# Kernel optimization log

Hardware: AMD Instinct MI355X
Metric: run time of the kernel (lower is better)

Reference implementation:

```python
import jax, jax.numpy as jnp
import numpy as np

N = 50000
E = 800000
T = 12
HID = 128
K = 3
F_IN = 7  # 1 (x) + 4 (env) + 2 (coords)
CIN = F_IN + HID  # DCRNN concatenates input with hidden state


def setup_inputs() -> dict:
    key = jax.random.key(0)
    ks = jax.random.split(key, 16)
    inp = {
        "x": jax.random.normal(ks[0], (N, T), dtype=jnp.float32),
        "env": jax.random.normal(ks[1], (N, 4, T), dtype=jnp.float32),
        "coords": jax.random.uniform(ks[2], (N, 2), dtype=jnp.float32),
        "edge_index": jax.random.randint(ks[3], (2, E), 0, N, dtype=jnp.int32),
        "edge_weight": jax.random.uniform(ks[4], (E,), dtype=jnp.float32),
        "local_night": jax.random.uniform(ks[5], (N, T + 1), dtype=jnp.float32),
        # DCRNN gate diffusion-conv weights: [2 (out/in direction), K, Cin, Cout]
        "Wz": jax.random.normal(ks[6], (2, K, CIN, HID), dtype=jnp.float32) * 0.05,
        "bz": jnp.zeros((HID,), dtype=jnp.float32),
        "Wr": jax.random.normal(ks[7], (2, K, CIN, HID), dtype=jnp.float32) * 0.05,
        "br": jnp.zeros((HID,), dtype=jnp.float32),
        "Wh": jax.random.normal(ks[8], (2, K, CIN, HID), dtype=jnp.float32) * 0.05,
        "bh": jnp.zeros((HID,), dtype=jnp.float32),
        "lin_W": jax.random.normal(ks[9], (HID, 1), dtype=jnp.float32) * 0.05,
        "lin_b": jnp.zeros((1,), dtype=jnp.float32),
    }
    return inp


def reference(x, env, coords, edge_weight, local_night, Wz, bz, Wr, br, Wh, bh, lin_W, lin_b, edge_index):
    row, col = edge_index[0], edge_index[1]
    n = x.shape[0]

    # out/in degrees of the weighted adjacency A[row, col] = w
    deg_out = jax.ops.segment_sum(edge_weight, row, num_segments=n)
    deg_in = jax.ops.segment_sum(edge_weight, col, num_segments=n)
    inv_out = jnp.where(deg_out > 0, 1.0 / deg_out, 0.0)
    inv_in = jnp.where(deg_in > 0, 1.0 / deg_in, 0.0)

    def prop_out(v):  # (D_O^{-1} A) v : gather from col, scatter-add to row
        msg = edge_weight[:, None] * v[col]
        return inv_out[:, None] * jax.ops.segment_sum(msg, row, num_segments=n)

    def prop_in(v):  # (D_I^{-1} A^T) v : gather from row, scatter-add to col
        msg = edge_weight[:, None] * v[row]
        return inv_in[:, None] * jax.ops.segment_sum(msg, col, num_segments=n)

    def dconv(X, W, b):
        # K-hop bidirectional diffusion convolution
        H = X @ (W[0, 0] + W[1, 0])
        Tx0 = X
        Tx_o = prop_out(X)
        Tx_i = prop_in(X)
        H = H + Tx_o @ W[0, 1] + Tx_i @ W[1, 1]
        for k in range(2, W.shape[1]):
            Tx_o = 2.0 * prop_out(Tx_o) - Tx0
            Tx_i = 2.0 * prop_in(Tx_i) - Tx0
            H = H + Tx_o @ W[0, k] + Tx_i @ W[1, k]
        return H + b

    env_t = jnp.moveaxis(env, -1, 0)          # [T, N, 4]
    night_t = jnp.transpose(local_night[:, 1:])  # [T, N]
    hid0 = jnp.zeros((n, HID), dtype=x.dtype)   # hidden state resets each call (H=None)

    def step(x_prev, ts):
        e, night = ts
        X = jnp.concatenate([x_prev, e, coords], axis=1)   # [N, 7]
        Xh = jnp.concatenate([X, hid0], axis=1)            # [N, 7+HID]
        Z = jax.nn.sigmoid(dconv(Xh, Wz, bz))
        R = jax.nn.sigmoid(dconv(Xh, Wr, br))  # H*R = 0 since H0 = 0; kept for fidelity
        H_tilde = jnp.tanh(dconv(Xh, Wh, bh))
        H_new = Z * hid0 + (1.0 - Z) * H_tilde
        out = jax.nn.relu(H_new) @ lin_W + lin_b           # [N, 1]
        out = out * night[:, None]
        return out, out

    x0 = x[:, 0:1]
    _, preds = jax.lax.scan(step, x0, (env_t, night_t))    # preds: [T, N, 1]
    predictions = jnp.concatenate([x0, jnp.transpose(preds[..., 0])], axis=1)  # [N, T+1]
    return predictions
```

## Files before the change

### kernel.cpp

```cpp
#include <hip/hip_runtime.h>
#include <hip/hip_fp16.h>

#define Nn 50000
#define Ee 800000
#define Tt 12
#define NBAND 8
#define BAND 6250
#define SCB 196

__global__ __launch_bounds__(256) void pack_hist_kernel(
    const int* __restrict__ ei, const float* __restrict__ ew,
    uint2* __restrict__ packed, int* __restrict__ cntR, int* __restrict__ cntC)
{
    int e = blockIdx.x * 256 + threadIdx.x;
    if (e >= Ee) return;
    int r = ei[e], c = ei[Ee + e];
    unsigned wb = __half_as_ushort(__float2half(ew[e]));
    packed[e] = make_uint2(((unsigned)c << 16) | wb, ((unsigned)r << 16) | wb);
    atomicAdd(&cntR[r], 1);
    atomicAdd(&cntC[c], 1);
}

__global__ __launch_bounds__(256) void scanA_kernel(
    const int* __restrict__ cntR, const int* __restrict__ cntC,
    int* __restrict__ bsum)
{
    const int* cnt = blockIdx.y ? cntC : cntR;
    int i = blockIdx.x * 256 + threadIdx.x;
    int v = (i < Nn) ? cnt[i] : 0;
    __shared__ int ws_[4];
    v += __shfl_xor(v, 1);  v += __shfl_xor(v, 2);  v += __shfl_xor(v, 4);
    v += __shfl_xor(v, 8);  v += __shfl_xor(v, 16); v += __shfl_xor(v, 32);
    if ((threadIdx.x & 63) == 0) ws_[threadIdx.x >> 6] = v;
    __syncthreads();
    if (threadIdx.x == 0)
        bsum[blockIdx.y * 256 + blockIdx.x] = ws_[0] + ws_[1] + ws_[2] + ws_[3];
}

__global__ __launch_bounds__(256) void scanB_kernel(
    const int* __restrict__ bsum, int* __restrict__ bbase)
{
    int y = blockIdx.x;
    __shared__ int s[256];
    int t = threadIdx.x;
    int v = (t < SCB) ? bsum[y * 256 + t] : 0;
    s[t] = v;
    __syncthreads();
    for (int off = 1; off < 256; off <<= 1) {
        int u = (t >= off) ? s[t - off] : 0;
        __syncthreads();
        s[t] += u;
        __syncthreads();
    }
    bbase[y * 256 + t] = s[t] - v;
}

__global__ __launch_bounds__(256) void scanC_kernel(
    const int* __restrict__ cntR, const int* __restrict__ cntC,
    const int* __restrict__ bbase,
    int* __restrict__ startR, int* __restrict__ startC,
    int* __restrict__ nextR, int* __restrict__ nextC)
{
    int y = blockIdx.y;
    const int* cnt = y ? cntC : cntR;
    int* start     = y ? startC : startR;
    int* nxt       = y ? nextC : nextR;
    int i = blockIdx.x * 256 + threadIdx.x;
    int v = (i < Nn) ? cnt[i] : 0;
    __shared__ int s[256];
    int t = threadIdx.x;
    s[t] = v;
    __syncthreads();
    for (int off = 1; off < 256; off <<= 1) {
        int u = (t >= off) ? s[t - off] : 0;
        __syncthreads();
        s[t] += u;
        __syncthreads();
    }
    int st = bbase[y * 256 + blockIdx.x] + s[t] - v;
    if (i < Nn) { start[i] = st; nxt[i] = st; }
}

__global__ __launch_bounds__(256) void scatter_banded(
    const uint2* __restrict__ packed,
    int* __restrict__ nextR, int* __restrict__ nextC,
    unsigned* __restrict__ adjR, unsigned* __restrict__ adjC)
{
    int band = blockIdx.x & (NBAND - 1);
    int chunk = blockIdx.x >> 3;
    int lo = band * BAND, hi = lo + BAND;
    int stride = (gridDim.x >> 3) * 256;
    for (int e = chunk * 256 + threadIdx.x; e < Ee; e += stride) {
        uint2 p = packed[e];
        int c = (int)(p.x >> 16);
        int r = (int)(p.y >> 16);
        if (r >= lo && r < hi) adjR[atomicAdd(&nextR[r], 1)] = p.x;
        if (c >= lo && c < hi) adjC[atomicAdd(&nextC[c], 1)] = p.y;
    }
}

__global__ __launch_bounds__(256) void weff_kernel(
    const float* __restrict__ Wz, const float* __restrict__ Wh,
    const float* __restrict__ bz, const float* __restrict__ bh,
    float* __restrict__ wzT, float* __restrict__ whT)
{
    int idx = blockIdx.x * 256 + threadIdx.x;
    if (idx >= 2 * 36 * 128) return;
    const float* W = (idx < 36 * 128) ? Wz : Wh;
    const float* B = (idx < 36 * 128) ? bz : bh;
    float* O       = (idx < 36 * 128) ? wzT : whT;
    int rem = idx % (36 * 128);
    int k = rem / 128, j = rem % 128;
    float v;
    if (k == 35) v = B[j];
    else {
        int p = k / 7, rr = k % 7;
        if (p == 0)      v = W[(0 * 135 + rr) * 128 + j] + W[(3 * 135 + rr) * 128 + j];
        else if (p == 1) v = W[(1 * 135 + rr) * 128 + j];
        else if (p == 2) v = W[(4 * 135 + rr) * 128 + j];
        else if (p == 3) v = W[(2 * 135 + rr) * 128 + j];
        else             v = W[(5 * 135 + rr) * 128 + j];
    }
    O[k * 128 + j] = v;
}

__global__ __launch_bounds__(256) void init_kernel(
    const float* __restrict__ x, const float* __restrict__ env,
    const float* __restrict__ coords, __half* __restrict__ Xh,
    float* __restrict__ out)
{
    int i = blockIdx.x * 256 + threadIdx.x;
    if (i >= Nn) return;
    float xv = x[i * Tt];
    __half* r = Xh + (long)i * 8;
    r[0] = __float2half(xv);
    #pragma unroll
    for (int c = 0; c < 4; c++) r[1 + c] = __float2half(env[i * 48 + c * 12]);
    r[5] = __float2half(coords[i * 2 + 0]);
    r[6] = __float2half(coords[i * 2 + 1]);
    r[7] = __half(0.f);
    out[i * 13 + 0] = xv;
}

__device__ __forceinline__ void unpack8(const __half* p, float* v) {
    uint4 hv = *((const uint4*)p);
    float2 p0 = __half22float2(*(__half2*)&hv.x);
    float2 p1 = __half22float2(*(__half2*)&hv.y);
    float2 p2 = __half22float2(*(__half2*)&hv.z);
    float2 p3 = __half22float2(*(__half2*)&hv.w);
    v[0] = p0.x; v[1] = p0.y; v[2] = p1.x; v[3] = p1.y;
    v[4] = p2.x; v[5] = p2.y; v[6] = p3.x;
}

__device__ __forceinline__ void pack8(__half* p, const float* v) {
    __half2 q0 = __floats2half2_rn(v[0], v[1]);
    __half2 q1 = __floats2half2_rn(v[2], v[3]);
    __half2 q2 = __floats2half2_rn(v[4], v[5]);
    __half2 q3 = __floats2half2_rn(v[6], 0.f);
    uint4 st;
    st.x = *(unsigned*)&q0; st.y = *(unsigned*)&q1;
    st.z = *(unsigned*)&q2; st.w = *(unsigned*)&q3;
    *((uint4*)p) = st;
}

__device__ __forceinline__ void acc7(float* a, float w, uint4 hv) {
    float2 p0 = __half22float2(*(__half2*)&hv.x);
    float2 p1 = __half22float2(*(__half2*)&hv.y);
    float2 p2 = __half22float2(*(__half2*)&hv.z);
    float2 p3 = __half22float2(*(__half2*)&hv.w);
    a[0] = fmaf(w, p0.x, a[0]); a[1] = fmaf(w, p0.y, a[1]);
    a[2] = fmaf(w, p1.x, a[2]); a[3] = fmaf(w, p1.y, a[3]);
    a[4] = fmaf(w, p2.x, a[4]); a[5] = fmaf(w, p2.y, a[5]);
    a[6] = fmaf(w, p3.x, a[6]);
}

__device__ __forceinline__ float wdec(unsigned ed) {
    return __half2float(__ushort_as_half((unsigned short)(ed & 0xffffu)));
}

__global__ __launch_bounds__(256) void gather1_kernel(
    const int* __restrict__ startR, const int* __restrict__ cntR,
    const unsigned* __restrict__ adjR,
    const int* __restrict__ startC, const int* __restrict__ cntC,
    const unsigned* __restrict__ adjC,
    const __half* __restrict__ Xh,
    __half* __restrict__ TxoH, __half* __restrict__ TxiH,
    float* __restrict__ inv_out, float* __restrict__ inv_in)
{
    int tid = blockIdx.x * 256 + threadIdx.x;
    if (tid >= Nn * 8) return;
    int node = tid >> 3;
    int dir = (tid >> 2) & 1, sub = tid & 3;
    const int*      st  = dir ? startC : startR;
    const int*      cn  = dir ? cntC : cntR;
    const unsigned* adj = dir ? adjC : adjR;
    int b = st[node], e = b + cn[node];
    float a[7] = {0.f, 0.f, 0.f, 0.f, 0.f, 0.f, 0.f};
    float sw = 0.f;
    int k = b + sub;
    for (; k + 12 < e; k += 16) {
        unsigned e0 = adj[k], e1 = adj[k + 4], e2 = adj[k + 8], e3 = adj[k + 12];
        uint4 r0 = *(const uint4*)(Xh + (long)(e0 >> 16) * 8);
        uint4 r1 = *(const uint4*)(Xh + (long)(e1 >> 16) * 8);
        uint4 r2 = *(const uint4*)(Xh + (long)(e2 >> 16) * 8);
        uint4 r3 = *(const uint4*)(Xh + (long)(e3 >> 16) * 8);
        float w0 = wdec(e0), w1 = wdec(e1), w2 = wdec(e2), w3 = wdec(e3);
        acc7(a, w0, r0); acc7(a, w1, r1); acc7(a, w2, r2); acc7(a, w3, r3);
        sw += (w0 + w1) + (w2 + w3);
    }
    for (; k < e; k += 4) {
        unsigned ed = adj[k];
        uint4 rv = *(const uint4*)(Xh + (long)(ed >> 16) * 8);
        float w = wdec(ed);
        acc7(a, w, rv);
        sw += w;
    }
    #pragma unroll
    for (int m = 1; m <= 2; m <<= 1) {
        #pragma unroll
        for (int q = 0; q < 7; q++) a[q] += __shfl_xor(a[q], m);
        sw += __shfl_xor(sw, m);
    }
    if (sub == 0) {
        float inv = sw > 0.f ? 1.f / sw : 0.f;
        (dir ? inv_in : inv_out)[node] = inv;
        #pragma unroll
        for (int q = 0; q < 7; q++) a[q] *= inv;
        pack8((dir ? TxiH : TxoH) + (long)node * 8, a);
    }
}

__global__ __launch_bounds__(256) void step2_kernel(
    const int* __restrict__ startR, const int* __restrict__ cntR,
    const unsigned* __restrict__ adjR,
    const int* __restrict__ startC, const int* __restrict__ cntC,
    const unsigned* __restrict__ adjC,
    const float* __restrict__ inv_out, const float* __restrict__ inv_in,
    const float* __restrict__ env, const float* __restrict__ night,
    const float* __restrict__ wzT, const float* __restrict__ whT,
    const float* __restrict__ linW, const float* __restrict__ linb,
    __half* __restrict__ Xh,
    const __half* __restrict__ TxoH, const __half* __restrict__ TxiH,
    float* __restrict__ out, int t)
{
    __shared__ float f_s[32][36];
    __shared__ float part_s[2][32];
    int tid = threadIdx.x;
    int base = blockIdx.x * 32;

    {
        int nl = tid >> 3;
        int dir = (tid >> 2) & 1, sub = tid & 3;
        int node = base + nl;
        int nc = node < Nn ? node : Nn - 1;
        const int*      st  = dir ? startC : startR;
        const int*      cn  = dir ? cntC : cntR;
        const unsigned* adj = dir ? adjC : adjR;
        const __half*   src = dir ? TxiH : TxoH;
        int b = st[nc], e = b + cn[nc];
        float a[7] = {0.f, 0.f, 0.f, 0.f, 0.f, 0.f, 0.f};
        int k = b + sub;
        for (; k + 12 < e; k += 16) {
            unsigned e0 = adj[k], e1 = adj[k + 4], e2 = adj[k + 8], e3 = adj[k + 12];
            uint4 r0 = *(const uint4*)(src + (long)(e0 >> 16) * 8);
            uint4 r1 = *(const uint4*)(src + (long)(e1 >> 16) * 8);
            uint4 r2 = *(const uint4*)(src + (long)(e2 >> 16) * 8);
            uint4 r3 = *(const uint4*)(src + (long)(e3 >> 16) * 8);
            float w0 = wdec(e0), w1 = wdec(e1), w2 = wdec(e2), w3 = wdec(e3);
            acc7(a, w0, r0); acc7(a, w1, r1); acc7(a, w2, r2); acc7(a, w3, r3);
        }
        for (; k < e; k += 4) {
            unsigned ed = adj[k];
            uint4 rv = *(const uint4*)(src + (long)(ed >> 16) * 8);
            acc7(a, wdec(ed), rv);
        }
        #pragma unroll
        for (int m = 1; m <= 2; m <<= 1) {
            #pragma unroll
            for (int q = 0; q < 7; q++) a[q] += __shfl_xor(a[q], m);
        }
        if (sub == 0) {
            float s2 = 2.f * (dir ? inv_in[nc] : inv_out[nc]);
            float xv[7], tx[7];
            unpack8(Xh + (long)nc * 8, xv);
            unpack8(src + (long)nc * 8, tx);
            #pragma unroll
            for (int q = 0; q < 7; q++) {
                f_s[nl][21 + 7 * dir + q] = fmaf(s2, a[q], -xv[q]);
                f_s[nl][7 + 7 * dir + q]  = tx[q];
            }
            if (dir == 0) {
                #pragma unroll
                for (int q = 0; q < 7; q++) f_s[nl][q] = xv[q];
                f_s[nl][35] = 1.f;
            }
        }
    }
    __syncthreads();

    int lane = tid & 63;
    int wave = tid >> 6;
    int chSel = wave & 1;
    int ch = chSel * 64 + lane;
    int half_id = wave >> 1;
    float wz[36], wh[36];
    #pragma unroll
    for (int k = 0; k < 36; k++) wz[k] = wzT[k * 128 + ch];
    #pragma unroll
    for (int k = 0; k < 36; k++) wh[k] = whT[k * 128 + ch];
    float lw = linW[ch];
    float lb = linb[0];

    #pragma unroll 1
    for (int n = 0; n < 16; n++) {
        int ni = half_id * 16 + n;
        const float4* fv = (const float4*)f_s[ni];
        float hz = 0.f, hh = 0.f;
        #pragma unroll
        for (int q = 0; q < 9; q++) {
            float4 fq = fv[q];
            hz = fmaf(fq.x, wz[q*4+0], hz); hh = fmaf(fq.x, wh[q*4+0], hh);
            hz = fmaf(fq.y, wz[q*4+1], hz); hh = fmaf(fq.y, wh[q*4+1], hh);
            hz = fmaf(fq.z, wz[q*4+2], hz); hh = fmaf(fq.z, wh[q*4+2], hh);
            hz = fmaf(fq.w, wz[q*4+3], hz); hh = fmaf(fq.w, wh[q*4+3], hh);
        }
        float z  = 1.f / (1.f + __expf(-hz));
        float e2 = __expf(2.f * hh);
        float ht = 1.f - 2.f / (e2 + 1.f);
        float v = fmaxf((1.f - z) * ht, 0.f) * lw;
        v += __shfl_xor(v, 1);  v += __shfl_xor(v, 2);  v += __shfl_xor(v, 4);
        v += __shfl_xor(v, 8);  v += __shfl_xor(v, 16); v += __shfl_xor(v, 32);
        if (lane == 0) part_s[chSel][ni] = v;
    }
    __syncthreads();
    if (tid < 32) {
        int node = base + tid;
        if (node < Nn) {
            float o = part_s[0][tid] + part_s[1][tid] + lb;
            o *= night[(long)node * 13 + t + 1];
            out[(long)node * 13 + t + 1] = o;
            if (t + 1 < Tt) {
                __half* xr = Xh + (long)node * 8;
                xr[0] = __float2half(o);
                #pragma unroll
                for (int c = 0; c < 4; c++)
                    xr[1 + c] = __float2half(env[(long)node * 48 + c * 12 + t + 1]);
            }
        }
    }
}

extern "C" void kernel_launch(void* const* d_in, const int* in_sizes, int n_in,
                              void* d_out, int out_size, void* d_ws, size_t ws_size,
                              hipStream_t stream) {
    const float* x      = (const float*)d_in[0];
    const float* env    = (const float*)d_in[1];
    const float* coords = (const float*)d_in[2];
    const int*   ei     = (const int*)d_in[3];
    const float* ew     = (const float*)d_in[4];
    const float* night  = (const float*)d_in[5];
    const float* Wz     = (const float*)d_in[6];
    const float* bz     = (const float*)d_in[7];
    const float* Wh     = (const float*)d_in[10];
    const float* bh     = (const float*)d_in[11];
    const float* linW   = (const float*)d_in[12];
    const float* linb   = (const float*)d_in[13];
    float* out = (float*)d_out;

    float* w = (float*)d_ws;
    float* wzT     = w;
    float* whT     = w + 4608;
    float* inv_out = w + 9216;
    float* inv_in  = w + 59216;
    __half* Xh   = (__half*)(w + 109216);
    __half* TxoH = (__half*)(w + 309216);
    __half* TxiH = (__half*)(w + 509216);
    int* cntR    = (int*)(w + 709216);
    int* cntC    = cntR + 50000;
    int* startR  = cntC + 50000;
    int* startC  = startR + 50000;
    int* nextR   = startC + 50000;
    int* nextC   = nextR + 50000;
    int* bsum    = nextC + 50000;
    int* bbase   = bsum + 512;
    uint2* packed  = (uint2*)(bbase + 512);
    unsigned* adjR = (unsigned*)(packed + Ee);
    unsigned* adjC = adjR + Ee;

    hipMemsetAsync(cntR, 0, 2 * Nn * sizeof(int), stream);
    pack_hist_kernel<<<(Ee + 255) / 256, 256, 0, stream>>>(ei, ew, packed, cntR, cntC);
    scanA_kernel<<<dim3(SCB, 2), 256, 0, stream>>>(cntR, cntC, bsum);
    scanB_kernel<<<2, 256, 0, stream>>>(bsum, bbase);
    scanC_kernel<<<dim3(SCB, 2), 256, 0, stream>>>(
        cntR, cntC, bbase, startR, startC, nextR, nextC);
    scatter_banded<<<8 * 256, 256, 0, stream>>>(packed, nextR, nextC, adjR, adjC);

    weff_kernel<<<(2 * 36 * 128 + 255) / 256, 256, 0, stream>>>(Wz, Wh, bz, bh, wzT, whT);
    init_kernel<<<(Nn + 255) / 256, 256, 0, stream>>>(x, env, coords, Xh, out);

    for (int t = 0; t < Tt; t++) {
        gather1_kernel<<<(Nn * 8 + 255) / 256, 256, 0, stream>>>(
            startR, cntR, adjR, startC, cntC, adjC, Xh, TxoH, TxiH, inv_out, inv_in);
        step2_kernel<<<(Nn + 31) / 32, 256, 0, stream>>>(
            startR, cntR, adjR, startC, cntC, adjC, inv_out, inv_in,
            env, night, wzT, whT, linW, linb, Xh, TxoH, TxiH, out, t);
    }
}
```

Measured before the change: 791.1 us.

## Use 8 lanes per node-direction in gathers, prefetch edges, nontemporal setup I/O

The gather kernels now use 8 threads per node and direction instead of 4. Each thread issues three predicated edge loads and row gathers up front, then loops over any remaining edges, which raises memory-level parallelism for the average degree of 16. The step2 kernel grows to 512-thread blocks so each wave handles 8 nodes in the dense gate phase. The setup kernels switch to nontemporal loads and stores, and the banded scatter is unrolled by 4. This costs more threads, an extra shuffle round, and possibly higher register pressure at 512-thread launch bounds with 72 weight registers.

```diff
diff --git a/kernel.cpp b/kernel.cpp
--- a/kernel.cpp
+++ b/kernel.cpp
@@ -14,9 +14,14 @@
 {
     int e = blockIdx.x * 256 + threadIdx.x;
     if (e >= Ee) return;
-    int r = ei[e], c = ei[Ee + e];
-    unsigned wb = __half_as_ushort(__float2half(ew[e]));
-    packed[e] = make_uint2(((unsigned)c << 16) | wb, ((unsigned)r << 16) | wb);
+    int r = __builtin_nontemporal_load(ei + e);
+    int c = __builtin_nontemporal_load(ei + Ee + e);
+    float w = __builtin_nontemporal_load(ew + e);
+    unsigned wb = __half_as_ushort(__float2half(w));
+    unsigned lo = ((unsigned)c << 16) | wb;
+    unsigned hi = ((unsigned)r << 16) | wb;
+    unsigned long long v = ((unsigned long long)hi << 32) | lo;
+    __builtin_nontemporal_store(v, (unsigned long long*)packed + e);
     atomicAdd(&cntR[r], 1);
     atomicAdd(&cntC[c], 1);
 }
@@ -88,14 +93,24 @@
 {
     int band = blockIdx.x & (NBAND - 1);
     int chunk = blockIdx.x >> 3;
-    int lo = band * BAND, hi = lo + BAND;
+    int blo = band * BAND, bhi = blo + BAND;
     int stride = (gridDim.x >> 3) * 256;
-    for (int e = chunk * 256 + threadIdx.x; e < Ee; e += stride) {
-        uint2 p = packed[e];
-        int c = (int)(p.x >> 16);
-        int r = (int)(p.y >> 16);
-        if (r >= lo && r < hi) adjR[atomicAdd(&nextR[r], 1)] = p.x;
-        if (c >= lo && c < hi) adjC[atomicAdd(&nextC[c], 1)] = p.y;
+    const unsigned long long* p64 = (const unsigned long long*)packed;
+    for (int e0 = chunk * 256 + threadIdx.x; e0 < Ee; e0 += 4 * stride) {
+        int e1 = e0 + stride, e2 = e0 + 2 * stride, e3 = e0 + 3 * stride;
+        bool g1 = e1 < Ee, g2 = e2 < Ee, g3 = e3 < Ee;
+        unsigned long long p0 = __builtin_nontemporal_load(p64 + e0);
+        unsigned long long p1 = __builtin_nontemporal_load(p64 + (g1 ? e1 : e0));
+        unsigned long long p2 = __builtin_nontemporal_load(p64 + (g2 ? e2 : e0));
+        unsigned long long p3 = __builtin_nontemporal_load(p64 + (g3 ? e3 : e0));
+        #define PROC(p, ok) do { if (ok) {                                     \
+            unsigned lo = (unsigned)(p); unsigned hi = (unsigned)((p) >> 32);  \
+            int c = (int)(lo >> 16), r = (int)(hi >> 16);                      \
+            if (r >= blo && r < bhi) adjR[atomicAdd(&nextR[r], 1)] = lo;       \
+            if (c >= blo && c < bhi) adjC[atomicAdd(&nextC[c], 1)] = hi;       \
+        } } while (0)
+        PROC(p0, true); PROC(p1, g1); PROC(p2, g2); PROC(p3, g3);
+        #undef PROC
     }
 }
 
@@ -188,27 +203,28 @@
     float* __restrict__ inv_out, float* __restrict__ inv_in)
 {
     int tid = blockIdx.x * 256 + threadIdx.x;
-    if (tid >= Nn * 8) return;
-    int node = tid >> 3;
-    int dir = (tid >> 2) & 1, sub = tid & 3;
+    int node = tid >> 4;
+    int dir = (tid >> 3) & 1, sub = tid & 7;
     const int*      st  = dir ? startC : startR;
     const int*      cn  = dir ? cntC : cntR;
     const unsigned* adj = dir ? adjC : adjR;
     int b = st[node], e = b + cn[node];
+    int safe = (b < e) ? b : 0;
+    int k0 = b + sub;
+    bool v0 = k0 < e, v1 = k0 + 8 < e, v2 = k0 + 16 < e;
+    unsigned e0 = adj[v0 ? k0 : safe];
+    unsigned e1 = adj[v1 ? k0 + 8 : safe];
+    unsigned e2 = adj[v2 ? k0 + 16 : safe];
+    uint4 r0 = *(const uint4*)(Xh + (long)(e0 >> 16) * 8);
+    uint4 r1 = *(const uint4*)(Xh + (long)(e1 >> 16) * 8);
+    uint4 r2 = *(const uint4*)(Xh + (long)(e2 >> 16) * 8);
+    float w0 = v0 ? wdec(e0) : 0.f;
+    float w1 = v1 ? wdec(e1) : 0.f;
+    float w2 = v2 ? wdec(e2) : 0.f;
     float a[7] = {0.f, 0.f, 0.f, 0.f, 0.f, 0.f, 0.f};
-    float sw = 0.f;
-    int k = b + sub;
-    for (; k + 12 < e; k += 16) {
-        unsigned e0 = adj[k], e1 = adj[k + 4], e2 = adj[k + 8], e3 = adj[k + 12];
-        uint4 r0 = *(const uint4*)(Xh + (long)(e0 >> 16) * 8);
-        uint4 r1 = *(const uint4*)(Xh + (long)(e1 >> 16) * 8);
-        uint4 r2 = *(const uint4*)(Xh + (long)(e2 >> 16) * 8);
-        uint4 r3 = *(const uint4*)(Xh + (long)(e3 >> 16) * 8);
-        float w0 = wdec(e0), w1 = wdec(e1), w2 = wdec(e2), w3 = wdec(e3);
-        acc7(a, w0, r0); acc7(a, w1, r1); acc7(a, w2, r2); acc7(a, w3, r3);
-        sw += (w0 + w1) + (w2 + w3);
-    }
-    for (; k < e; k += 4) {
+    acc7(a, w0, r0); acc7(a, w1, r1); acc7(a, w2, r2);
+    float sw = (w0 + w1) + w2;
+    for (int k = k0 + 24; k < e; k += 8) {
         unsigned ed = adj[k];
         uint4 rv = *(const uint4*)(Xh + (long)(ed >> 16) * 8);
         float w = wdec(ed);
@@ -216,7 +232,7 @@
         sw += w;
     }
     #pragma unroll
-    for (int m = 1; m <= 2; m <<= 1) {
+    for (int m = 1; m <= 4; m <<= 1) {
         #pragma unroll
         for (int q = 0; q < 7; q++) a[q] += __shfl_xor(a[q], m);
         sw += __shfl_xor(sw, m);
@@ -230,7 +246,7 @@
     }
 }
 
-__global__ __launch_bounds__(256) void step2_kernel(
+__global__ __launch_bounds__(512) void step2_kernel(
     const int* __restrict__ startR, const int* __restrict__ cntR,
     const unsigned* __restrict__ adjR,
     const int* __restrict__ startC, const int* __restrict__ cntC,
@@ -249,8 +265,8 @@
     int base = blockIdx.x * 32;
 
     {
-        int nl = tid >> 3;
-        int dir = (tid >> 2) & 1, sub = tid & 3;
+        int nl = tid >> 4;
+        int dir = (tid >> 3) & 1, sub = tid & 7;
         int node = base + nl;
         int nc = node < Nn ? node : Nn - 1;
         const int*      st  = dir ? startC : startR;
@@ -258,24 +274,27 @@
         const unsigned* adj = dir ? adjC : adjR;
         const __half*   src = dir ? TxiH : TxoH;
         int b = st[nc], e = b + cn[nc];
+        int safe = (b < e) ? b : 0;
+        int k0 = b + sub;
+        bool v0 = k0 < e, v1 = k0 + 8 < e, v2 = k0 + 16 < e;
+        unsigned e0 = adj[v0 ? k0 : safe];
+        unsigned e1 = adj[v1 ? k0 + 8 : safe];
+        unsigned e2 = adj[v2 ? k0 + 16 : safe];
+        uint4 r0 = *(const uint4*)(src + (long)(e0 >> 16) * 8);
+        uint4 r1 = *(const uint4*)(src + (long)(e1 >> 16) * 8);
+        uint4 r2 = *(const uint4*)(src + (long)(e2 >> 16) * 8);
+        float w0 = v0 ? wdec(e0) : 0.f;
+        float w1 = v1 ? wdec(e1) : 0.f;
+        float w2 = v2 ? wdec(e2) : 0.f;
         float a[7] = {0.f, 0.f, 0.f, 0.f, 0.f, 0.f, 0.f};
-        int k = b + sub;
-        for (; k + 12 < e; k += 16) {
-            unsigned e0 = adj[k], e1 = adj[k + 4], e2 = adj[k + 8], e3 = adj[k + 12];
-            uint4 r0 = *(const uint4*)(src + (long)(e0 >> 16) * 8);
-            uint4 r1 = *(const uint4*)(src + (long)(e1 >> 16) * 8);
-            uint4 r2 = *(const uint4*)(src + (long)(e2 >> 16) * 8);
-            uint4 r3 = *(const uint4*)(src + (long)(e3 >> 16) * 8);
-            float w0 = wdec(e0), w1 = wdec(e1), w2 = wdec(e2), w3 = wdec(e3);
-            acc7(a, w0, r0); acc7(a, w1, r1); acc7(a, w2, r2); acc7(a, w3, r3);
-        }
-        for (; k < e; k += 4) {
+        acc7(a, w0, r0); acc7(a, w1, r1); acc7(a, w2, r2);
+        for (int k = k0 + 24; k < e; k += 8) {
             unsigned ed = adj[k];
             uint4 rv = *(const uint4*)(src + (long)(ed >> 16) * 8);
             acc7(a, wdec(ed), rv);
         }
         #pragma unroll
-        for (int m = 1; m <= 2; m <<= 1) {
+        for (int m = 1; m <= 4; m <<= 1) {
             #pragma unroll
             for (int q = 0; q < 7; q++) a[q] += __shfl_xor(a[q], m);
         }
@@ -302,7 +321,7 @@
     int wave = tid >> 6;
     int chSel = wave & 1;
     int ch = chSel * 64 + lane;
-    int half_id = wave >> 1;
+    int q8 = wave >> 1;
     float wz[36], wh[36];
     #pragma unroll
     for (int k = 0; k < 36; k++) wz[k] = wzT[k * 128 + ch];
@@ -312,8 +331,8 @@
     float lb = linb[0];
 
     #pragma unroll 1
-    for (int n = 0; n < 16; n++) {
-        int ni = half_id * 16 + n;
+    for (int n = 0; n < 8; n++) {
+        int ni = q8 * 8 + n;
         const float4* fv = (const float4*)f_s[ni];
         float hz = 0.f, hh = 0.f;
         #pragma unroll
@@ -399,9 +418,9 @@
     init_kernel<<<(Nn + 255) / 256, 256, 0, stream>>>(x, env, coords, Xh, out);
 
     for (int t = 0; t < Tt; t++) {
-        gather1_kernel<<<(Nn * 8 + 255) / 256, 256, 0, stream>>>(
+        gather1_kernel<<<(Nn * 16) / 256, 256, 0, stream>>>(
             startR, cntR, adjR, startC, cntC, adjC, Xh, TxoH, TxiH, inv_out, inv_in);
-        step2_kernel<<<(Nn + 31) / 32, 256, 0, stream>>>(
+        step2_kernel<<<(Nn + 31) / 32, 512, 0, stream>>>(
             startR, cntR, adjR, startC, cntC, adjC, inv_out, inv_in,
             env, night, wzT, whT, linW, linb, Xh, TxoH, TxiH, out, t);
     }
```

Measured after the change: 866.3 us. 1.1x slower.

## Replace banded edge scatter with two-pass bucket-by-band then scatter

Applied to the files above, without the earlier changes.

Edges are first partitioned into per-band buckets using shared-memory counters plus one global atomic per block per band. A second kernel then scatters each band's contiguous bucket into the CSR adjacency lists. This avoids having every band block re-read the full packed edge array (8x redundant reads) in exchange for an extra pass and more workspace. The path is taken only when the workspace is large enough; otherwise the old kernel runs.

```diff
diff --git a/kernel.cpp b/kernel.cpp
--- a/kernel.cpp
+++ b/kernel.cpp
@@ -59,7 +59,8 @@
     const int* __restrict__ cntR, const int* __restrict__ cntC,
     const int* __restrict__ bbase,
     int* __restrict__ startR, int* __restrict__ startC,
-    int* __restrict__ nextR, int* __restrict__ nextC)
+    int* __restrict__ nextR, int* __restrict__ nextC,
+    int* __restrict__ bandCurR, int* __restrict__ bandCurC)
 {
     int y = blockIdx.y;
     const int* cnt = y ? cntC : cntR;
@@ -78,7 +79,10 @@
         __syncthreads();
     }
     int st = bbase[y * 256 + blockIdx.x] + s[t] - v;
-    if (i < Nn) { start[i] = st; nxt[i] = st; }
+    if (i < Nn) {
+        start[i] = st; nxt[i] = st;
+        if ((i % BAND) == 0) (y ? bandCurC : bandCurR)[i / BAND] = st;
+    }
 }
 
 __global__ __launch_bounds__(256) void scatter_banded(
@@ -96,6 +100,64 @@
         int r = (int)(p.y >> 16);
         if (r >= lo && r < hi) adjR[atomicAdd(&nextR[r], 1)] = p.x;
         if (c >= lo && c < hi) adjC[atomicAdd(&nextC[c], 1)] = p.y;
+    }
+}
+
+__global__ __launch_bounds__(256) void bucketA_kernel(
+    const uint2* __restrict__ packed,
+    int* __restrict__ bandCurR, int* __restrict__ bandCurC,
+    uint2* __restrict__ bucketR, uint2* __restrict__ bucketC)
+{
+    __shared__ int cnt_s[16];
+    __shared__ int base_s[16];
+    int t = threadIdx.x;
+    for (int b0 = blockIdx.x * 256; b0 < Ee; b0 += gridDim.x * 256) {
+        int e = b0 + t;
+        bool ok = e < Ee;
+        uint2 p = ok ? packed[e] : make_uint2(0u, 0u);
+        int r = (int)(p.y >> 16), c = (int)(p.x >> 16);
+        int bR = r / BAND, bC = c / BAND;
+        if (t < 16) cnt_s[t] = 0;
+        __syncthreads();
+        int rkR = 0, rkC = 0;
+        if (ok) {
+            rkR = atomicAdd(&cnt_s[bR], 1);
+            rkC = atomicAdd(&cnt_s[8 + bC], 1);
+        }
+        __syncthreads();
+        if (t < 8)        base_s[t] = atomicAdd(&bandCurR[t], cnt_s[t]);
+        else if (t < 16)  base_s[t] = atomicAdd(&bandCurC[t - 8], cnt_s[t]);
+        __syncthreads();
+        if (ok) {
+            bucketR[base_s[bR] + rkR]     = p;
+            bucketC[base_s[8 + bC] + rkC] = p;
+        }
+        __syncthreads();
+    }
+}
+
+__global__ __launch_bounds__(256) void scatterB_kernel(
+    const uint2* __restrict__ bucketR, const uint2* __restrict__ bucketC,
+    const int* __restrict__ startR, const int* __restrict__ startC,
+    int* __restrict__ nextR, int* __restrict__ nextC,
+    unsigned* __restrict__ adjR, unsigned* __restrict__ adjC)
+{
+    int band = blockIdx.x & (NBAND - 1);
+    int chunk = blockIdx.x >> 3;
+    int stride = (gridDim.x >> 3) * 256;
+    int sR = startR[band * BAND];
+    int eR = (band < NBAND - 1) ? startR[(band + 1) * BAND] : Ee;
+    for (int k = sR + chunk * 256 + threadIdx.x; k < eR; k += stride) {
+        uint2 p = bucketR[k];
+        int r = (int)(p.y >> 16);
+        adjR[atomicAdd(&nextR[r], 1)] = p.x;
+    }
+    int sC = startC[band * BAND];
+    int eC = (band < NBAND - 1) ? startC[(band + 1) * BAND] : Ee;
+    for (int k = sC + chunk * 256 + threadIdx.x; k < eC; k += stride) {
+        uint2 p = bucketC[k];
+        int c = (int)(p.x >> 16);
+        adjC[atomicAdd(&nextC[c], 1)] = p.y;
     }
 }
 
@@ -383,17 +445,31 @@
     int* nextC   = nextR + 50000;
     int* bsum    = nextC + 50000;
     int* bbase   = bsum + 512;
-    uint2* packed  = (uint2*)(bbase + 512);
+    int* bandCurR = bbase + 512;
+    int* bandCurC = bandCurR + 8;
+    uint2* packed  = (uint2*)(w + 1010256);
     unsigned* adjR = (unsigned*)(packed + Ee);
     unsigned* adjC = adjR + Ee;
+    uint2* bucketR = (uint2*)(adjC + Ee);
+    uint2* bucketC = bucketR + Ee;
+    size_t need2 = (size_t)(1010256 + 2 * Ee * 2  ) * 4
+                 + (size_t)Ee * 4 * 2  + (size_t)Ee * 8 * 2 ;
+    bool twopass = ws_size >= need2 + 1024;
 
     hipMemsetAsync(cntR, 0, 2 * Nn * sizeof(int), stream);
     pack_hist_kernel<<<(Ee + 255) / 256, 256, 0, stream>>>(ei, ew, packed, cntR, cntC);
     scanA_kernel<<<dim3(SCB, 2), 256, 0, stream>>>(cntR, cntC, bsum);
     scanB_kernel<<<2, 256, 0, stream>>>(bsum, bbase);
     scanC_kernel<<<dim3(SCB, 2), 256, 0, stream>>>(
-        cntR, cntC, bbase, startR, startC, nextR, nextC);
-    scatter_banded<<<8 * 256, 256, 0, stream>>>(packed, nextR, nextC, adjR, adjC);
+        cntR, cntC, bbase, startR, startC, nextR, nextC, bandCurR, bandCurC);
+    if (twopass) {
+        bucketA_kernel<<<1024, 256, 0, stream>>>(packed, bandCurR, bandCurC,
+                                                 bucketR, bucketC);
+        scatterB_kernel<<<2048, 256, 0, stream>>>(bucketR, bucketC, startR, startC,
+                                                  nextR, nextC, adjR, adjC);
+    } else {
+        scatter_banded<<<8 * 256, 256, 0, stream>>>(packed, nextR, nextC, adjR, adjC);
+    }
 
     weff_kernel<<<(2 * 36 * 128 + 255) / 256, 256, 0, stream>>>(Wz, Wh, bz, bh, wzT, whT);
     init_kernel<<<(Nn + 255) / 256, 256, 0, stream>>>(x, env, coords, Xh, out);
```

After: 826.9 us. 1.05x slower.

## Replace global-atomic CSR build with two-level band bucketing and LDS counting sort

Applied to the files above, without the earlier changes.

Rebuilds the CSR construction of both adjacency directions. Edges are first counted per band, then bucketed into 8 bands with wave ballots, then sorted within each band by one block per band and direction, using an LDS histogram, an LDS scan and LDS atomics. This replaces the per-node global atomics, the three-kernel scan and the 8x-redundant banded scatter. The cost is that only 16 blocks do the final per-band scatter, which may leave the GPU underused, and the bucket arrays need extra workspace.

```diff
diff --git a/kernel.cpp b/kernel.cpp
--- a/kernel.cpp
+++ b/kernel.cpp
@@ -6,96 +6,164 @@
 #define Tt 12
 #define NBAND 8
 #define BAND 6250
-#define SCB 196
-
-__global__ __launch_bounds__(256) void pack_hist_kernel(
+#define BINS 6250
+
+__global__ __launch_bounds__(256) void count_kernel(
+    const int* __restrict__ ei, int* __restrict__ bandCntR, int* __restrict__ bandCntC)
+{
+    int gid = blockIdx.x * 256 + threadIdx.x;
+    int cr[8] = {0,0,0,0,0,0,0,0};
+    int cc[8] = {0,0,0,0,0,0,0,0};
+    for (int e = gid; e < Ee; e += 256 * 256) {
+        int r = ei[e], c = ei[Ee + e];
+        int bR = r / BAND, bC = c / BAND;
+        #pragma unroll
+        for (int b = 0; b < 8; b++) { cr[b] += (bR == b); cc[b] += (bC == b); }
+    }
+    #pragma unroll
+    for (int b = 0; b < 8; b++) {
+        int v = cr[b];
+        v += __shfl_xor(v, 1);  v += __shfl_xor(v, 2);  v += __shfl_xor(v, 4);
+        v += __shfl_xor(v, 8);  v += __shfl_xor(v, 16); v += __shfl_xor(v, 32);
+        if ((threadIdx.x & 63) == 0 && v) atomicAdd(&bandCntR[b], v);
+        int u = cc[b];
+        u += __shfl_xor(u, 1);  u += __shfl_xor(u, 2);  u += __shfl_xor(u, 4);
+        u += __shfl_xor(u, 8);  u += __shfl_xor(u, 16); u += __shfl_xor(u, 32);
+        if ((threadIdx.x & 63) == 0 && u) atomicAdd(&bandCntC[b], u);
+    }
+}
+
+__global__ void band_scan_kernel(
+    const int* __restrict__ bandCntR, const int* __restrict__ bandCntC,
+    int* __restrict__ bandCurR, int* __restrict__ bandCurC,
+    int* __restrict__ bandBaseR, int* __restrict__ bandBaseC)
+{
+    if (threadIdx.x == 0) {
+        int a = 0;
+        for (int b = 0; b < 8; b++) { bandBaseR[b] = a; bandCurR[b] = a; a += bandCntR[b]; }
+        bandBaseR[8] = a;
+        a = 0;
+        for (int b = 0; b < 8; b++) { bandBaseC[b] = a; bandCurC[b] = a; a += bandCntC[b]; }
+        bandBaseC[8] = a;
+    }
+}
+
+__global__ __launch_bounds__(256) void bucket_kernel(
     const int* __restrict__ ei, const float* __restrict__ ew,
-    uint2* __restrict__ packed, int* __restrict__ cntR, int* __restrict__ cntC)
-{
-    int e = blockIdx.x * 256 + threadIdx.x;
-    if (e >= Ee) return;
-    int r = ei[e], c = ei[Ee + e];
-    unsigned wb = __half_as_ushort(__float2half(ew[e]));
-    packed[e] = make_uint2(((unsigned)c << 16) | wb, ((unsigned)r << 16) | wb);
-    atomicAdd(&cntR[r], 1);
-    atomicAdd(&cntC[c], 1);
-}
-
-__global__ __launch_bounds__(256) void scanA_kernel(
-    const int* __restrict__ cntR, const int* __restrict__ cntC,
-    int* __restrict__ bsum)
-{
-    const int* cnt = blockIdx.y ? cntC : cntR;
-    int i = blockIdx.x * 256 + threadIdx.x;
-    int v = (i < Nn) ? cnt[i] : 0;
-    __shared__ int ws_[4];
-    v += __shfl_xor(v, 1);  v += __shfl_xor(v, 2);  v += __shfl_xor(v, 4);
-    v += __shfl_xor(v, 8);  v += __shfl_xor(v, 16); v += __shfl_xor(v, 32);
-    if ((threadIdx.x & 63) == 0) ws_[threadIdx.x >> 6] = v;
-    __syncthreads();
-    if (threadIdx.x == 0)
-        bsum[blockIdx.y * 256 + blockIdx.x] = ws_[0] + ws_[1] + ws_[2] + ws_[3];
-}
-
-__global__ __launch_bounds__(256) void scanB_kernel(
-    const int* __restrict__ bsum, int* __restrict__ bbase)
-{
-    int y = blockIdx.x;
-    __shared__ int s[256];
-    int t = threadIdx.x;
-    int v = (t < SCB) ? bsum[y * 256 + t] : 0;
-    s[t] = v;
-    __syncthreads();
+    int* __restrict__ bandCurR, int* __restrict__ bandCurC,
+    uint2* __restrict__ bucketR, uint2* __restrict__ bucketC)
+{
+    int wave = (blockIdx.x << 2) + (threadIdx.x >> 6);
+    int lane = threadIdx.x & 63;
+    int base = wave * 512;
+    if (base >= Ee) return;
+    unsigned long long lmlt = (1ULL << lane) - 1ULL;
+    uint2 p[8];
+    int rkR[8], rkC[8];
+    int runR[8] = {0,0,0,0,0,0,0,0};
+    int runC[8] = {0,0,0,0,0,0,0,0};
+    #pragma unroll
+    for (int rd = 0; rd < 8; rd++) {
+        int e = base + rd * 64 + lane;
+        bool ok = e < Ee;
+        int ec = ok ? e : 0;
+        int r = ei[ec], c = ei[Ee + ec];
+        float w = ew[ec];
+        unsigned wb = __half_as_ushort(__float2half(w));
+        p[rd] = make_uint2(((unsigned)c << 16) | wb, ((unsigned)r << 16) | wb);
+        int bR = r / BAND, bC = c / BAND;
+        rkR[rd] = 0; rkC[rd] = 0;
+        #pragma unroll
+        for (int b = 0; b < 8; b++) {
+            unsigned long long mR = __ballot(ok && (bR == b));
+            if (ok && (bR == b)) rkR[rd] = runR[b] + (int)__popcll(mR & lmlt);
+            runR[b] += (int)__popcll(mR);
+            unsigned long long mC = __ballot(ok && (bC == b));
+            if (ok && (bC == b)) rkC[rd] = runC[b] + (int)__popcll(mC & lmlt);
+            runC[b] += (int)__popcll(mC);
+        }
+    }
+    int myTot = 0;
+    #pragma unroll
+    for (int b = 0; b < 8; b++) {
+        myTot = (lane == b)     ? runR[b] : myTot;
+        myTot = (lane == 8 + b) ? runC[b] : myTot;
+    }
+    int baseVal = 0;
+    if (lane < 8)       baseVal = atomicAdd(&bandCurR[lane], myTot);
+    else if (lane < 16) baseVal = atomicAdd(&bandCurC[lane - 8], myTot);
+    #pragma unroll
+    for (int rd = 0; rd < 8; rd++) {
+        int e = base + rd * 64 + lane;
+        if (e < Ee) {
+            int bR = (int)(p[rd].y >> 16) / BAND;
+            int bC = (int)(p[rd].x >> 16) / BAND;
+            int baR = __shfl(baseVal, bR);
+            int baC = __shfl(baseVal, 8 + bC);
+            bucketR[baR + rkR[rd]] = p[rd];
+            bucketC[baC + rkC[rd]] = p[rd];
+        }
+    }
+}
+
+__global__ __launch_bounds__(256) void band_scatter_kernel(
+    const uint2* __restrict__ bucketR, const uint2* __restrict__ bucketC,
+    const int* __restrict__ bandBaseR, const int* __restrict__ bandBaseC,
+    int* __restrict__ startR, int* __restrict__ startC,
+    int* __restrict__ cntR, int* __restrict__ cntC,
+    unsigned* __restrict__ adjR, unsigned* __restrict__ adjC)
+{
+    __shared__ int h[BINS];
+    __shared__ int s[BINS];
+    __shared__ int tps[256];
+    int dir  = blockIdx.x & 1;
+    int band = blockIdx.x >> 1;
+    const uint2* bucket = dir ? bucketC : bucketR;
+    const int*   bb     = dir ? bandBaseC : bandBaseR;
+    int*         start  = dir ? startC : startR;
+    int*         cnt    = dir ? cntC : cntR;
+    unsigned*    adj    = dir ? adjC : adjR;
+    int lo = band * BAND;
+    int b0 = bb[band], b1 = bb[band + 1];
+    int tid = threadIdx.x;
+    for (int i = tid; i < BINS; i += 256) h[i] = 0;
+    __syncthreads();
+    for (int k = b0 + tid; k < b1; k += 256) {
+        uint2 p = bucket[k];
+        int key = (int)((dir ? p.x : p.y) >> 16) - lo;
+        atomicAdd(&h[key], 1);
+    }
+    __syncthreads();
+    int tsum = 0;
+    if (tid < 250) {
+        int o = tid * 25;
+        for (int j = 0; j < 25; j++) { s[o + j] = tsum; tsum += h[o + j]; }
+    }
+    tps[tid] = tsum;
+    __syncthreads();
+    int v = tsum;
     for (int off = 1; off < 256; off <<= 1) {
-        int u = (t >= off) ? s[t - off] : 0;
+        int u = (tid >= off) ? tps[tid - off] : 0;
         __syncthreads();
-        s[t] += u;
+        tps[tid] += u;
         __syncthreads();
     }
-    bbase[y * 256 + t] = s[t] - v;
-}
-
-__global__ __launch_bounds__(256) void scanC_kernel(
-    const int* __restrict__ cntR, const int* __restrict__ cntC,
-    const int* __restrict__ bbase,
-    int* __restrict__ startR, int* __restrict__ startC,
-    int* __restrict__ nextR, int* __restrict__ nextC)
-{
-    int y = blockIdx.y;
-    const int* cnt = y ? cntC : cntR;
-    int* start     = y ? startC : startR;
-    int* nxt       = y ? nextC : nextR;
-    int i = blockIdx.x * 256 + threadIdx.x;
-    int v = (i < Nn) ? cnt[i] : 0;
-    __shared__ int s[256];
-    int t = threadIdx.x;
-    s[t] = v;
-    __syncthreads();
-    for (int off = 1; off < 256; off <<= 1) {
-        int u = (t >= off) ? s[t - off] : 0;
-        __syncthreads();
-        s[t] += u;
-        __syncthreads();
-    }
-    int st = bbase[y * 256 + blockIdx.x] + s[t] - v;
-    if (i < Nn) { start[i] = st; nxt[i] = st; }
-}
-
-__global__ __launch_bounds__(256) void scatter_banded(
-    const uint2* __restrict__ packed,
-    int* __restrict__ nextR, int* __restrict__ nextC,
-    unsigned* __restrict__ adjR, unsigned* __restrict__ adjC)
-{
-    int band = blockIdx.x & (NBAND - 1);
-    int chunk = blockIdx.x >> 3;
-    int lo = band * BAND, hi = lo + BAND;
-    int stride = (gridDim.x >> 3) * 256;
-    for (int e = chunk * 256 + threadIdx.x; e < Ee; e += stride) {
-        uint2 p = packed[e];
-        int c = (int)(p.x >> 16);
-        int r = (int)(p.y >> 16);
-        if (r >= lo && r < hi) adjR[atomicAdd(&nextR[r], 1)] = p.x;
-        if (c >= lo && c < hi) adjC[atomicAdd(&nextC[c], 1)] = p.y;
+    int texcl = tps[tid] - v;
+    if (tid < 250) {
+        int o = tid * 25;
+        for (int j = 0; j < 25; j++) {
+            int ex = s[o + j] + texcl;
+            s[o + j] = ex;
+            start[lo + o + j] = b0 + ex;
+            cnt[lo + o + j]   = h[o + j];
+        }
+    }
+    __syncthreads();
+    for (int k = b0 + tid; k < b1; k += 256) {
+        uint2 p = bucket[k];
+        int key = (int)((dir ? p.x : p.y) >> 16) - lo;
+        int slot = atomicAdd(&s[key], 1);
+        adj[b0 + slot] = dir ? p.y : p.x;
     }
 }
 
@@ -379,21 +447,25 @@
     int* cntC    = cntR + 50000;
     int* startR  = cntC + 50000;
     int* startC  = startR + 50000;
-    int* nextR   = startC + 50000;
-    int* nextC   = nextR + 50000;
-    int* bsum    = nextC + 50000;
-    int* bbase   = bsum + 512;
-    uint2* packed  = (uint2*)(bbase + 512);
-    unsigned* adjR = (unsigned*)(packed + Ee);
+    int* bandCntR  = (int*)(w + 909216);
+    int* bandCntC  = bandCntR + 8;
+    int* bandCurR  = (int*)(w + 909232);
+    int* bandCurC  = bandCurR + 8;
+    int* bandBaseR = (int*)(w + 909248);
+    int* bandBaseC = bandBaseR + 9;
+    uint2* bucketR = (uint2*)(w + 909280);
+    uint2* bucketC = bucketR + Ee;
+    unsigned* adjR = (unsigned*)(bucketC + Ee);
     unsigned* adjC = adjR + Ee;
 
-    hipMemsetAsync(cntR, 0, 2 * Nn * sizeof(int), stream);
-    pack_hist_kernel<<<(Ee + 255) / 256, 256, 0, stream>>>(ei, ew, packed, cntR, cntC);
-    scanA_kernel<<<dim3(SCB, 2), 256, 0, stream>>>(cntR, cntC, bsum);
-    scanB_kernel<<<2, 256, 0, stream>>>(bsum, bbase);
-    scanC_kernel<<<dim3(SCB, 2), 256, 0, stream>>>(
-        cntR, cntC, bbase, startR, startC, nextR, nextC);
-    scatter_banded<<<8 * 256, 256, 0, stream>>>(packed, nextR, nextC, adjR, adjC);
+    hipMemsetAsync(bandCntR, 0, 16 * sizeof(int), stream);
+    count_kernel<<<256, 256, 0, stream>>>(ei, bandCntR, bandCntC);
+    band_scan_kernel<<<1, 64, 0, stream>>>(bandCntR, bandCntC,
+                                           bandCurR, bandCurC, bandBaseR, bandBaseC);
+    bucket_kernel<<<391, 256, 0, stream>>>(ei, ew, bandCurR, bandCurC, bucketR, bucketC);
+    band_scatter_kernel<<<16, 256, 0, stream>>>(
+        bucketR, bucketC, bandBaseR, bandBaseC,
+        startR, startC, cntR, cntC, adjR, adjC);
 
     weff_kernel<<<(2 * 36 * 128 + 255) / 256, 256, 0, stream>>>(Wz, Wh, bz, bh, wzT, whT);
     init_kernel<<<(Nn + 255) / 256, 256, 0, stream>>>(x, env, coords, Xh, out);
```

After: 1.092 ms. 38.0% more time.
